# Performance work log

Hardware: AMD Instinct MI355X
Metric: run time of the kernel (lower is better)

The kernel has to match this reference:

```python
import jax, jax.numpy as jnp
import numpy as np

N = 100000
E = 3200000
D_IN = 128
D_OUT = 128
ALPHA = 0.2  # LeakyReLU negative slope
LN_EPS = 1e-5


def setup_inputs() -> dict:
    key = jax.random.key(0)
    k1, k2, k3, k4, k5 = jax.random.split(key, 5)
    x = jax.random.normal(k1, (N, D_IN), dtype=jnp.float32)
    edge = jax.random.randint(k2, (2, E), 0, N, dtype=jnp.int64)
    # Linear params (kaiming-normal-ish init)
    W = jax.random.normal(k3, (D_OUT, D_IN), dtype=jnp.float32) * np.sqrt(2.0 / D_IN)
    b = jnp.zeros((D_OUT,), dtype=jnp.float32)
    # attention vector a: (2*out,)
    a = jax.random.normal(k4, (2 * D_OUT,), dtype=jnp.float32) * np.sqrt(2.0 / (2 * D_OUT))
    ln_w = jnp.ones((D_OUT,), dtype=jnp.float32)
    ln_b = jnp.zeros((D_OUT,), dtype=jnp.float32)
    return {"x": x, "W": W, "b": b, "a": a, "ln_w": ln_w, "ln_b": ln_b, "edge": edge}


def reference(x, W, b, a, ln_w, ln_b, edge):
    n = x.shape[0]
    d_out = W.shape[0]
    h = x @ W.T + b  # [N, D_OUT]
    src, dst = edge[0], edge[1]
    # a.mm(cat(h[src], h[dst]).T) == h[src] @ a1 + h[dst] @ a2
    a1, a2 = a[:d_out], a[d_out:]
    node_s1 = h @ a1  # [N]
    node_s2 = h @ a2  # [N]
    z = node_s1[src] + node_s2[dst]  # [E]
    edge_e = jnp.exp(-jax.nn.leaky_relu(z, ALPHA))  # [E]
    # sparse spmm: h_prime[i] = sum_{e: src=i} edge_e[e] * h[dst[e]]
    msgs = edge_e[:, None] * h[dst]  # [E, D_OUT]
    h_prime = jax.ops.segment_sum(msgs, src, num_segments=n)  # [N, D_OUT]
    # LayerNorm over last dim
    mu = jnp.mean(h_prime, axis=-1, keepdims=True)
    var = jnp.mean(jnp.square(h_prime - mu), axis=-1, keepdims=True)
    h_norm = (h_prime - mu) * jax.lax.rsqrt(var + LN_EPS) * ln_w + ln_b
    return jax.nn.elu(h_norm)
```

## Files before the change

kernel.cpp:

```cpp
#include <hip/hip_runtime.h>
#include <math.h>

#define D 128
#define GAT_ALPHA 0.2f
#define LN_EPS 1e-5f
#define NBMAX 1600
#define CAP 2400
#define ECHUNK 16384
#define XPITCH 136

typedef __attribute__((ext_vector_type(8))) short short8;
typedef __attribute__((ext_vector_type(4))) float floatx4;

__device__ __forceinline__ unsigned short f2bf(float f) {
    unsigned u = __float_as_uint(f);
    unsigned r = (u + 0x7fffu + ((u >> 16) & 1u)) >> 16;
    return (unsigned short)r;
}
__device__ __forceinline__ float bfl(unsigned u) { return __uint_as_float(u << 16); }
__device__ __forceinline__ float bfh(unsigned u) { return __uint_as_float(u & 0xffff0000u); }

__global__ __launch_bounds__(256) void prep_bfrag(const float* __restrict__ W,
                                                  unsigned short* __restrict__ Bfrag)
{
    for (int idx = threadIdx.x; idx < 2048; idx += 256) {
        int lane = idx & 63, ntkt = idx >> 6;
        int nt = ntkt >> 2, kt = ntkt & 3;
        int l16 = lane & 15, quad = lane >> 4;
        const float* wp = W + (size_t)(nt * 16 + l16) * D + kt * 32 + quad * 8;
        unsigned short* op = Bfrag + (size_t)idx * 8;
#pragma unroll
        for (int j = 0; j < 8; ++j) op[j] = f2bf(wp[j]);
    }
}

__global__ __launch_bounds__(256) void gemm_mfma(const float* __restrict__ x,
                                                 const unsigned short* __restrict__ Bfrag_g,
                                                 const float* __restrict__ b,
                                                 const float* __restrict__ a,
                                                 unsigned short* __restrict__ h16,
                                                 float* __restrict__ s1,
                                                 float* __restrict__ s2, int n)
{
    __shared__ unsigned short Bf[16384];
    __shared__ unsigned short xs[64 * XPITCH];
    const int tid = threadIdx.x;
    {
        const uint2* sp = (const uint2*)Bfrag_g;
        uint2* dp = (uint2*)Bf;
        for (int i = tid; i < 4096; i += 256) dp[i] = sp[i];
    }
    const int lane = tid & 63, wave = tid >> 6;
    const int l16 = lane & 15, quad = lane >> 4;
    const int row0 = blockIdx.x * 64;

    for (int i = tid; i < 2048; i += 256) {
        int row = i >> 5, c4 = i & 31;
        float4 v = make_float4(0.f, 0.f, 0.f, 0.f);
        if (row0 + row < n) v = *(const float4*)(x + (size_t)(row0 + row) * D + c4 * 4);
        ushort4 o;
        o.x = f2bf(v.x); o.y = f2bf(v.y); o.z = f2bf(v.z); o.w = f2bf(v.w);
        *(ushort4*)&xs[row * XPITCH + c4 * 4] = o;
    }

    float bcol[8], a1c[8], a2c[8];
#pragma unroll
    for (int nt = 0; nt < 8; ++nt) {
        int c = nt * 16 + l16;
        bcol[nt] = b[c]; a1c[nt] = a[c]; a2c[nt] = a[D + c];
    }
    __syncthreads();

    floatx4 acc[8];
#pragma unroll
    for (int nt = 0; nt < 8; ++nt) acc[nt] = (floatx4){0.f, 0.f, 0.f, 0.f};

#pragma unroll
    for (int kt = 0; kt < 4; ++kt) {
        short8 af = *(const short8*)&xs[(wave * 16 + l16) * XPITCH + kt * 32 + quad * 8];
#pragma unroll
        for (int nt = 0; nt < 8; ++nt) {
            short8 bf = *(const short8*)&Bf[(size_t)((nt * 4 + kt) * 64 + lane) * 8];
            acc[nt] = __builtin_amdgcn_mfma_f32_16x16x32_bf16(af, bf, acc[nt], 0, 0, 0);
        }
    }

    float hv[4][8];
#pragma unroll
    for (int r = 0; r < 4; ++r) {
        float p1 = 0.f, p2 = 0.f;
#pragma unroll
        for (int nt = 0; nt < 8; ++nt) {
            float v = acc[nt][r] + bcol[nt];
            hv[r][nt] = v;
            p1 = fmaf(v, a1c[nt], p1);
            p2 = fmaf(v, a2c[nt], p2);
        }
#pragma unroll
        for (int off = 8; off > 0; off >>= 1) {
            p1 += __shfl_xor(p1, off);
            p2 += __shfl_xor(p2, off);
        }
        int crow = row0 + wave * 16 + quad * 4 + r;
        if (crow < n && l16 == 0) { s1[crow] = p1; s2[crow] = p2; }
    }

    __syncthreads();
#pragma unroll
    for (int r = 0; r < 4; ++r)
#pragma unroll
        for (int nt = 0; nt < 8; ++nt)
            xs[(wave * 16 + quad * 4 + r) * XPITCH + nt * 16 + l16] = f2bf(hv[r][nt]);
    __syncthreads();

    for (int i = tid; i < 1024; i += 256) {
        int row = i >> 4, c = i & 15;
        if (row0 + row < n)
            *(uint4*)(h16 + (size_t)(row0 + row) * D + c * 8) =
                *(const uint4*)&xs[row * XPITCH + c * 8];
    }
}

__global__ __launch_bounds__(512) void partition_kernel(const int* __restrict__ src,
                                                        const int* __restrict__ dst,
                                                        int* __restrict__ gcnt,
                                                        int* __restrict__ pairs,
                                                        int nE, int nb)
{
    __shared__ int cnt[NBMAX], basex[NBMAX], cnt2x[NBMAX];
    int tid = threadIdx.x;
    for (int i = tid; i < nb; i += 512) { cnt[i] = 0; cnt2x[i] = 0; }
    __syncthreads();
    int e0 = blockIdx.x * ECHUNK;
    int e1 = e0 + ECHUNK; if (e1 > nE) e1 = nE;
    for (int e = e0 + tid; e < e1; e += 512)
        atomicAdd(&cnt[src[e] >> 6], 1);
    __syncthreads();
    for (int i = tid; i < nb; i += 512)
        basex[i] = cnt[i] ? atomicAdd(&gcnt[i], cnt[i]) : 0;
    __syncthreads();
    for (int e = e0 + tid; e < e1; e += 512) {
        int s = src[e];
        int bb = s >> 6;
        int l = basex[bb] + atomicAdd(&cnt2x[bb], 1);
        if (l < CAP) pairs[(size_t)bb * CAP + l] = ((s & 63) << 24) | dst[e];
    }
}

__global__ __launch_bounds__(256, 8) void sort_aggregate(const int* __restrict__ pairs,
                                                         const int* __restrict__ gcnt,
                                                         const float* __restrict__ s1,
                                                         const float* __restrict__ s2,
                                                         const unsigned short* __restrict__ h16,
                                                         const float* __restrict__ ln_w,
                                                         const float* __restrict__ ln_b,
                                                         float* __restrict__ out, int n)
{
    __shared__ int2 csr2[CAP];
    __shared__ int cnt[64], cnt2[64], excl[65];
    __shared__ float sA[64];

    const int bkt = blockIdx.x, tid = threadIdx.x;
    const size_t base = (size_t)bkt * CAP;
    int m = gcnt[bkt]; if (m > CAP) m = CAP;

    if (tid < 64) {
        cnt[tid] = 0; cnt2[tid] = 0;
        int node = bkt * 64 + tid;
        sA[tid] = (node < n) ? s1[node] : 0.f;
    }
    __syncthreads();

    for (int e = tid; e < m; e += 256)
        atomicAdd(&cnt[((unsigned)pairs[base + e]) >> 24], 1);
    __syncthreads();

    if (tid < 64) {
        int v = cnt[tid], incl = v;
#pragma unroll
        for (int off = 1; off < 64; off <<= 1) {
            int t = __shfl_up(incl, off);
            if (tid >= off) incl += t;
        }
        excl[tid] = incl - v;
        if (tid == 63) excl[64] = incl;
    }
    __syncthreads();

    for (int e = tid; e < m; e += 256) {
        int w = pairs[base + e];
        int sl = ((unsigned)w) >> 24;
        int d = w & 0xFFFFFF;
        float z = sA[sl] + s2[d];
        float lz = z > 0.f ? z : GAT_ALPHA * z;
        float ee = __expf(-lz);
        int pos = excl[sl] + atomicAdd(&cnt2[sl], 1);
        csr2[pos] = make_int2(d, __float_as_int(ee));
    }
    __syncthreads();

    const int lane = tid & 63, wv = tid >> 6;
    const int q = lane >> 4, l16 = lane & 15;

    for (int i = 0; i < 16; ++i) {
        int nl = wv * 16 + i;
        int node = bkt * 64 + nl;
        if (node >= n) break;
        int e0 = excl[nl], e1 = excl[nl + 1];

        float acc[8];
#pragma unroll
        for (int j = 0; j < 8; ++j) acc[j] = 0.f;

        int e = e0 + q;
        for (; e + 12 < e1; e += 16) {
            int2 pa = csr2[e];
            int2 pb = csr2[e + 4];
            int2 pc = csr2[e + 8];
            int2 pd = csr2[e + 12];
            uint4 ua = *(const uint4*)(h16 + (size_t)pa.x * D + l16 * 8);
            uint4 ub = *(const uint4*)(h16 + (size_t)pb.x * D + l16 * 8);
            uint4 uc = *(const uint4*)(h16 + (size_t)pc.x * D + l16 * 8);
            uint4 ud = *(const uint4*)(h16 + (size_t)pd.x * D + l16 * 8);
            float ea = __int_as_float(pa.y);
            float eb = __int_as_float(pb.y);
            float ec = __int_as_float(pc.y);
            float ed = __int_as_float(pd.y);
            acc[0] = fmaf(ea, bfl(ua.x), acc[0]);
            acc[1] = fmaf(ea, bfh(ua.x), acc[1]);
            acc[2] = fmaf(ea, bfl(ua.y), acc[2]);
            acc[3] = fmaf(ea, bfh(ua.y), acc[3]);
            acc[4] = fmaf(ea, bfl(ua.z), acc[4]);
            acc[5] = fmaf(ea, bfh(ua.z), acc[5]);
            acc[6] = fmaf(ea, bfl(ua.w), acc[6]);
            acc[7] = fmaf(ea, bfh(ua.w), acc[7]);
            acc[0] = fmaf(eb, bfl(ub.x), acc[0]);
            acc[1] = fmaf(eb, bfh(ub.x), acc[1]);
            acc[2] = fmaf(eb, bfl(ub.y), acc[2]);
            acc[3] = fmaf(eb, bfh(ub.y), acc[3]);
            acc[4] = fmaf(eb, bfl(ub.z), acc[4]);
            acc[5] = fmaf(eb, bfh(ub.z), acc[5]);
            acc[6] = fmaf(eb, bfl(ub.w), acc[6]);
            acc[7] = fmaf(eb, bfh(ub.w), acc[7]);
            acc[0] = fmaf(ec, bfl(uc.x), acc[0]);
            acc[1] = fmaf(ec, bfh(uc.x), acc[1]);
            acc[2] = fmaf(ec, bfl(uc.y), acc[2]);
            acc[3] = fmaf(ec, bfh(uc.y), acc[3]);
            acc[4] = fmaf(ec, bfl(uc.z), acc[4]);
            acc[5] = fmaf(ec, bfh(uc.z), acc[5]);
            acc[6] = fmaf(ec, bfl(uc.w), acc[6]);
            acc[7] = fmaf(ec, bfh(uc.w), acc[7]);
            acc[0] = fmaf(ed, bfl(ud.x), acc[0]);
            acc[1] = fmaf(ed, bfh(ud.x), acc[1]);
            acc[2] = fmaf(ed, bfl(ud.y), acc[2]);
            acc[3] = fmaf(ed, bfh(ud.y), acc[3]);
            acc[4] = fmaf(ed, bfl(ud.z), acc[4]);
            acc[5] = fmaf(ed, bfh(ud.z), acc[5]);
            acc[6] = fmaf(ed, bfl(ud.w), acc[6]);
            acc[7] = fmaf(ed, bfh(ud.w), acc[7]);
        }
        for (; e < e1; e += 4) {
            int2 p = csr2[e];
            float ee = __int_as_float(p.y);
            uint4 u = *(const uint4*)(h16 + (size_t)p.x * D + l16 * 8);
            acc[0] = fmaf(ee, bfl(u.x), acc[0]);
            acc[1] = fmaf(ee, bfh(u.x), acc[1]);
            acc[2] = fmaf(ee, bfl(u.y), acc[2]);
            acc[3] = fmaf(ee, bfh(u.y), acc[3]);
            acc[4] = fmaf(ee, bfl(u.z), acc[4]);
            acc[5] = fmaf(ee, bfh(u.z), acc[5]);
            acc[6] = fmaf(ee, bfl(u.w), acc[6]);
            acc[7] = fmaf(ee, bfh(u.w), acc[7]);
        }
#pragma unroll
        for (int j = 0; j < 8; ++j) acc[j] += __shfl_down(acc[j], 32);
#pragma unroll
        for (int j = 0; j < 8; ++j) acc[j] += __shfl_down(acc[j], 16);

        float sum = 0.f, sq = 0.f;
#pragma unroll
        for (int j = 0; j < 8; ++j) { sum += acc[j]; sq += acc[j] * acc[j]; }
#pragma unroll
        for (int off = 8; off > 0; off >>= 1) {
            sum += __shfl_xor(sum, off);
            sq  += __shfl_xor(sq, off);
        }

        if (q == 0) {
            float mu   = sum * (1.0f / 128.0f);
            float var  = sq * (1.0f / 128.0f) - mu * mu;
            float rstd = rsqrtf(var + LN_EPS);

            float4 w0 = *(const float4*)(ln_w + l16 * 8);
            float4 w1 = *(const float4*)(ln_w + l16 * 8 + 4);
            float4 b0 = *(const float4*)(ln_b + l16 * 8);
            float4 b1 = *(const float4*)(ln_b + l16 * 8 + 4);
            float y[8];
            y[0] = (acc[0] - mu) * rstd * w0.x + b0.x;
            y[1] = (acc[1] - mu) * rstd * w0.y + b0.y;
            y[2] = (acc[2] - mu) * rstd * w0.z + b0.z;
            y[3] = (acc[3] - mu) * rstd * w0.w + b0.w;
            y[4] = (acc[4] - mu) * rstd * w1.x + b1.x;
            y[5] = (acc[5] - mu) * rstd * w1.y + b1.y;
            y[6] = (acc[6] - mu) * rstd * w1.z + b1.z;
            y[7] = (acc[7] - mu) * rstd * w1.w + b1.w;
#pragma unroll
            for (int j = 0; j < 8; ++j) y[j] = y[j] > 0.f ? y[j] : expm1f(y[j]);
            float* op = out + (size_t)node * D + l16 * 8;
            *(float4*)op       = make_float4(y[0], y[1], y[2], y[3]);
            *(float4*)(op + 4) = make_float4(y[4], y[5], y[6], y[7]);
        }
    }
}

extern "C" void kernel_launch(void* const* d_in, const int* in_sizes, int n_in,
                              void* d_out, int out_size, void* d_ws, size_t ws_size,
                              hipStream_t stream)
{
    const float* x    = (const float*)d_in[0];
    const float* W    = (const float*)d_in[1];
    const float* b    = (const float*)d_in[2];
    const float* a    = (const float*)d_in[3];
    const float* ln_w = (const float*)d_in[4];
    const float* ln_b = (const float*)d_in[5];
    const int*   edge = (const int*)d_in[6];

    const int n  = in_sizes[0] / D;
    const int nE = in_sizes[6] / 2;
    const int* src = edge;
    const int* dst = edge + nE;
    const int nb2 = (n + 63) >> 6;

    float* out = (float*)d_out;

    unsigned short* h16 = (unsigned short*)d_ws;
    float* s1   = (float*)(h16 + (size_t)n * D);
    float* s2   = s1 + n;
    unsigned short* Bfrag = (unsigned short*)(s2 + n);
    int* pairs  = (int*)(Bfrag + 16384);
    int* gcnt   = pairs + (size_t)nb2 * CAP;

    hipMemsetAsync(gcnt, 0, (size_t)nb2 * sizeof(int), stream);

    prep_bfrag      <<<1, 256, 0, stream>>>(W, Bfrag);
    gemm_mfma       <<<(n + 63) / 64, 256, 0, stream>>>(x, Bfrag, b, a, h16, s1, s2, n);
    partition_kernel<<<(nE + ECHUNK - 1) / ECHUNK, 512, 0, stream>>>(src, dst, gcnt, pairs, nE, nb2);
    sort_aggregate  <<<nb2, 256, 0, stream>>>(pairs, gcnt, s1, s2, h16, ln_w, ln_b, out, n);
}
```

Before: 360.1 us.

## Fuse GEMM and edge partition into one launch and shrink buckets to 32 nodes

Merges the bf16 MFMA GEMM and the edge partitioning into a single kernel. Block ranges pick the role, and the shared memory is a union of the two roles' buffers. GEMM blocks grow to 512 threads covering 128 rows. Buckets shrink from 64 to 32 source nodes, so the aggregate kernel runs twice as many 128-thread blocks with a smaller CSR buffer, aiming for more parallelism and occupancy. The aim is to drop a launch and overlap the two independent phases. The risks are larger shared memory per block in the fused kernel and tighter per-bucket capacity (1280), which could drop edges for high-degree buckets.

```diff
diff --git a/kernel.cpp b/kernel.cpp
--- a/kernel.cpp
+++ b/kernel.cpp
@@ -4,8 +4,10 @@
 #define D 128
 #define GAT_ALPHA 0.2f
 #define LN_EPS 1e-5f
-#define NBMAX 1600
-#define CAP 2400
+#define BSHIFT 5
+#define BKT 32
+#define NBMAX 3200
+#define CAPB 1280
 #define ECHUNK 16384
 #define XPITCH 136
 
@@ -34,27 +36,55 @@
     }
 }
 
-__global__ __launch_bounds__(256) void gemm_mfma(const float* __restrict__ x,
-                                                 const unsigned short* __restrict__ Bfrag_g,
-                                                 const float* __restrict__ b,
-                                                 const float* __restrict__ a,
-                                                 unsigned short* __restrict__ h16,
-                                                 float* __restrict__ s1,
-                                                 float* __restrict__ s2, int n)
+union SmemU {
+    struct { unsigned short Bf[16384]; unsigned short xs[128 * XPITCH]; } g;
+    struct { int cnt[NBMAX]; int basex[NBMAX]; int cnt2x[NBMAX]; } p;
+};
+
+__global__ __launch_bounds__(512) void gemm_partition(
+        const float* __restrict__ x, const unsigned short* __restrict__ Bfrag_g,
+        const float* __restrict__ b, const float* __restrict__ a,
+        const int* __restrict__ src, const int* __restrict__ dst,
+        int* __restrict__ gcnt, int* __restrict__ pairs,
+        unsigned short* __restrict__ h16, float* __restrict__ s1,
+        float* __restrict__ s2, int n, int nE, int nb, int npart)
 {
-    __shared__ unsigned short Bf[16384];
-    __shared__ unsigned short xs[64 * XPITCH];
+    __shared__ SmemU sm;
     const int tid = threadIdx.x;
+
+    if (blockIdx.x < npart) {
+        int* cnt = sm.p.cnt; int* basex = sm.p.basex; int* cnt2x = sm.p.cnt2x;
+        for (int i = tid; i < nb; i += 512) { cnt[i] = 0; cnt2x[i] = 0; }
+        __syncthreads();
+        int e0 = blockIdx.x * ECHUNK;
+        int e1 = e0 + ECHUNK; if (e1 > nE) e1 = nE;
+        for (int e = e0 + tid; e < e1; e += 512)
+            atomicAdd(&cnt[src[e] >> BSHIFT], 1);
+        __syncthreads();
+        for (int i = tid; i < nb; i += 512)
+            basex[i] = cnt[i] ? atomicAdd(&gcnt[i], cnt[i]) : 0;
+        __syncthreads();
+        for (int e = e0 + tid; e < e1; e += 512) {
+            int s = src[e];
+            int bb = s >> BSHIFT;
+            int l = basex[bb] + atomicAdd(&cnt2x[bb], 1);
+            if (l < CAPB) pairs[(size_t)bb * CAPB + l] = ((s & (BKT - 1)) << 24) | dst[e];
+        }
+        return;
+    }
+
+    unsigned short* Bf = sm.g.Bf;
+    unsigned short* xs = sm.g.xs;
     {
         const uint2* sp = (const uint2*)Bfrag_g;
         uint2* dp = (uint2*)Bf;
-        for (int i = tid; i < 4096; i += 256) dp[i] = sp[i];
+        for (int i = tid; i < 4096; i += 512) dp[i] = sp[i];
     }
     const int lane = tid & 63, wave = tid >> 6;
     const int l16 = lane & 15, quad = lane >> 4;
-    const int row0 = blockIdx.x * 64;
-
-    for (int i = tid; i < 2048; i += 256) {
+    const int row0 = (blockIdx.x - npart) * 128;
+
+    for (int i = tid; i < 4096; i += 512) {
         int row = i >> 5, c4 = i & 31;
         float4 v = make_float4(0.f, 0.f, 0.f, 0.f);
         if (row0 + row < n) v = *(const float4*)(x + (size_t)(row0 + row) * D + c4 * 4);
@@ -113,7 +143,7 @@
             xs[(wave * 16 + quad * 4 + r) * XPITCH + nt * 16 + l16] = f2bf(hv[r][nt]);
     __syncthreads();
 
-    for (int i = tid; i < 1024; i += 256) {
+    for (int i = tid; i < 2048; i += 512) {
         int row = i >> 4, c = i & 15;
         if (row0 + row < n)
             *(uint4*)(h16 + (size_t)(row0 + row) * D + c * 8) =
@@ -121,33 +151,7 @@
     }
 }
 
-__global__ __launch_bounds__(512) void partition_kernel(const int* __restrict__ src,
-                                                        const int* __restrict__ dst,
-                                                        int* __restrict__ gcnt,
-                                                        int* __restrict__ pairs,
-                                                        int nE, int nb)
-{
-    __shared__ int cnt[NBMAX], basex[NBMAX], cnt2x[NBMAX];
-    int tid = threadIdx.x;
-    for (int i = tid; i < nb; i += 512) { cnt[i] = 0; cnt2x[i] = 0; }
-    __syncthreads();
-    int e0 = blockIdx.x * ECHUNK;
-    int e1 = e0 + ECHUNK; if (e1 > nE) e1 = nE;
-    for (int e = e0 + tid; e < e1; e += 512)
-        atomicAdd(&cnt[src[e] >> 6], 1);
-    __syncthreads();
-    for (int i = tid; i < nb; i += 512)
-        basex[i] = cnt[i] ? atomicAdd(&gcnt[i], cnt[i]) : 0;
-    __syncthreads();
-    for (int e = e0 + tid; e < e1; e += 512) {
-        int s = src[e];
-        int bb = s >> 6;
-        int l = basex[bb] + atomicAdd(&cnt2x[bb], 1);
-        if (l < CAP) pairs[(size_t)bb * CAP + l] = ((s & 63) << 24) | dst[e];
-    }
-}
-
-__global__ __launch_bounds__(256, 8) void sort_aggregate(const int* __restrict__ pairs,
+__global__ __launch_bounds__(128, 6) void sort_aggregate(const int* __restrict__ pairs,
                                                          const int* __restrict__ gcnt,
                                                          const float* __restrict__ s1,
                                                          const float* __restrict__ s2,
@@ -156,38 +160,38 @@
                                                          const float* __restrict__ ln_b,
                                                          float* __restrict__ out, int n)
 {
-    __shared__ int2 csr2[CAP];
-    __shared__ int cnt[64], cnt2[64], excl[65];
-    __shared__ float sA[64];
+    __shared__ int2 csr2[CAPB];
+    __shared__ int cnt[BKT], cnt2[BKT], excl[BKT + 1];
+    __shared__ float sA[BKT];
 
     const int bkt = blockIdx.x, tid = threadIdx.x;
-    const size_t base = (size_t)bkt * CAP;
-    int m = gcnt[bkt]; if (m > CAP) m = CAP;
-
-    if (tid < 64) {
+    const size_t base = (size_t)bkt * CAPB;
+    int m = gcnt[bkt]; if (m > CAPB) m = CAPB;
+
+    if (tid < BKT) {
         cnt[tid] = 0; cnt2[tid] = 0;
-        int node = bkt * 64 + tid;
+        int node = bkt * BKT + tid;
         sA[tid] = (node < n) ? s1[node] : 0.f;
     }
     __syncthreads();
 
-    for (int e = tid; e < m; e += 256)
+    for (int e = tid; e < m; e += 128)
         atomicAdd(&cnt[((unsigned)pairs[base + e]) >> 24], 1);
     __syncthreads();
 
-    if (tid < 64) {
+    if (tid < 32) {
         int v = cnt[tid], incl = v;
 #pragma unroll
-        for (int off = 1; off < 64; off <<= 1) {
+        for (int off = 1; off < 32; off <<= 1) {
             int t = __shfl_up(incl, off);
             if (tid >= off) incl += t;
         }
         excl[tid] = incl - v;
-        if (tid == 63) excl[64] = incl;
-    }
-    __syncthreads();
-
-    for (int e = tid; e < m; e += 256) {
+        if (tid == 31) excl[32] = incl;
+    }
+    __syncthreads();
+
+    for (int e = tid; e < m; e += 128) {
         int w = pairs[base + e];
         int sl = ((unsigned)w) >> 24;
         int d = w & 0xFFFFFF;
@@ -204,7 +208,7 @@
 
     for (int i = 0; i < 16; ++i) {
         int nl = wv * 16 + i;
-        int node = bkt * 64 + nl;
+        int node = bkt * BKT + nl;
         if (node >= n) break;
         int e0 = excl[nl], e1 = excl[nl + 1];
 
@@ -329,7 +333,9 @@
     const int nE = in_sizes[6] / 2;
     const int* src = edge;
     const int* dst = edge + nE;
-    const int nb2 = (n + 63) >> 6;
+    const int nb = (n + BKT - 1) >> BSHIFT;
+    const int npart = (nE + ECHUNK - 1) / ECHUNK;
+    const int ngemm = (n + 127) / 128;
 
     float* out = (float*)d_out;
 
@@ -338,12 +344,13 @@
     float* s2   = s1 + n;
     unsigned short* Bfrag = (unsigned short*)(s2 + n);
     int* pairs  = (int*)(Bfrag + 16384);
-    int* gcnt   = pairs + (size_t)nb2 * CAP;
-
-    hipMemsetAsync(gcnt, 0, (size_t)nb2 * sizeof(int), stream);
-
-    prep_bfrag      <<<1, 256, 0, stream>>>(W, Bfrag);
-    gemm_mfma       <<<(n + 63) / 64, 256, 0, stream>>>(x, Bfrag, b, a, h16, s1, s2, n);
-    partition_kernel<<<(nE + ECHUNK - 1) / ECHUNK, 512, 0, stream>>>(src, dst, gcnt, pairs, nE, nb2);
-    sort_aggregate  <<<nb2, 256, 0, stream>>>(pairs, gcnt, s1, s2, h16, ln_w, ln_b, out, n);
-}
+    int* gcnt   = pairs + (size_t)nb * CAPB;
+
+    hipMemsetAsync(gcnt, 0, (size_t)nb * sizeof(int), stream);
+
+    prep_bfrag    <<<1, 256, 0, stream>>>(W, Bfrag);
+    gemm_partition<<<npart + ngemm, 512, 0, stream>>>(x, Bfrag, b, a, src, dst,
+                                                      gcnt, pairs, h16, s1, s2,
+                                                      n, nE, nb, npart);
+    sort_aggregate<<<nb, 128, 0, stream>>>(pairs, gcnt, s1, s2, h16, ln_w, ln_b, out, n);
+}
```

After: 328.3 us. -8.8%, faster.
